# Kernel tuning notes

Measured on AMD Instinct MI355X. Metric: run time of the kernel, lower is better.

Reference implementation:

```python
import jax, jax.numpy as jnp
import numpy as np

N_NODES = 100000
N_EDGES = 800000
IN_DIM, HID_DIM, OUT_DIM = 128, 256, 40


def setup_inputs() -> dict:
    key = jax.random.key(0)
    ks = jax.random.split(key, 8)
    x = jax.random.normal(ks[0], (N_NODES, IN_DIM), dtype=jnp.float32)
    edge_index = jax.random.randint(ks[1], (2, N_EDGES), 0, N_NODES, dtype=jnp.int64)
    # PyG SAGEConv params: lin_l (neighbor path, with bias), lin_r (root path, no bias)
    def glorot(k, fan_in, fan_out):
        lim = np.sqrt(6.0 / (fan_in + fan_out)).astype(np.float32)
        return jax.random.uniform(k, (fan_in, fan_out), jnp.float32, -lim, lim)
    W1l = glorot(ks[2], IN_DIM, HID_DIM)
    W1r = glorot(ks[3], IN_DIM, HID_DIM)
    b1 = jnp.zeros((HID_DIM,), jnp.float32)
    W2l = glorot(ks[4], HID_DIM, OUT_DIM)
    W2r = glorot(ks[5], HID_DIM, OUT_DIM)
    b2 = jnp.zeros((OUT_DIM,), jnp.float32)
    return {"x": x, "edge_index": edge_index, "W1l": W1l, "b1": b1, "W1r": W1r,
            "W2l": W2l, "b2": b2, "W2r": W2r}


def _sage_conv(x, src, dst, Wl, b, Wr, n_nodes):
    # mean aggregation of neighbor features: gather x[src], scatter-add to dst, divide by degree
    msg = x[src]                                              # [E, D]
    agg = jax.ops.segment_sum(msg, dst, num_segments=n_nodes)  # [N, D]
    cnt = jax.ops.segment_sum(jnp.ones((src.shape[0],), x.dtype), dst,
                              num_segments=n_nodes)            # [N]
    agg = agg / jnp.maximum(cnt, 1.0)[:, None]
    # out = lin_l(mean_agg) + lin_r(x)  (lin_l carries the bias in PyG)
    return agg @ Wl + b + x @ Wr


def reference(x, edge_index, W1l, b1, W1r, W2l, b2, W2r):
    src, dst = edge_index[0], edge_index[1]
    n = x.shape[0]
    h = _sage_conv(x, src, dst, W1l, b1, W1r, n)
    h = jax.nn.relu(h)
    # F.dropout(training=self.training): identity at inference
    out = _sage_conv(h, src, dst, W2l, b2, W2r, n)
    return out
```

## Files before the change

### kernel.cpp

```cpp
#include <hip/hip_runtime.h>
#include <hip/hip_bf16.h>


#define NN   100000
#define NNP  100096
#define NE   800000
#define NB1  391
#define NCHK 32
#define ECH  25000
#define NSLI 16
#define NSL  6250

typedef unsigned short ushortT;
typedef __attribute__((ext_vector_type(8))) short bf16x8;
typedef __attribute__((ext_vector_type(4))) float f32x4;

__device__ __forceinline__ unsigned short f2b(float f) {
    unsigned u = __float_as_uint(f);
    return (unsigned short)((u + 0x7fffu + ((u >> 16) & 1u)) >> 16);
}
__device__ __forceinline__ float b2f(unsigned short v) {
    return __uint_as_float(((unsigned)v) << 16);
}
__device__ __forceinline__ void llds16(const unsigned short* g, unsigned short* s) {
    __builtin_amdgcn_global_load_lds(
        (const __attribute__((address_space(1))) void*)g,
        (__attribute__((address_space(3))) void*)s, 16, 0, 0);
}
__device__ __forceinline__ int fragIdx(int n, int k) {
    return (((n >> 4) * 8 + (k >> 5)) * 64 + ((k >> 3) & 3) * 16 + (n & 15)) * 8
           + (k & 7);
}

__global__ __launch_bounds__(256) void k_prep(
        const float* __restrict__ x,
        const float* __restrict__ W1l, const float* __restrict__ W1r,
        const float* __restrict__ W2l, const float* __restrict__ W2r,
        ushortT* __restrict__ Ac, ushortT* __restrict__ WT1f,
        ushortT* __restrict__ WT2f,
        const int* __restrict__ dst, int* __restrict__ deg32) {
    __shared__ int hist[NSL];
    int bid = blockIdx.x;
    if (bid < 12500) {
        int t = bid * 256 + threadIdx.x;
        int row = t >> 5, c4 = t & 31;
        float4 v = *(const float4*)&x[(size_t)row * 128 + c4 * 4];
        ushort4 o;
        o.x = f2b(v.x); o.y = f2b(v.y); o.z = f2b(v.z); o.w = f2b(v.w);
        *(ushort4*)(Ac + (size_t)row * 256 + 128 + c4 * 4) = o;

        if (t < 65536) {
            int n = t >> 8, k = t & 255;
            float w = (k < 128) ? W1l[(size_t)k * 256 + n]
                                : W1r[(size_t)(k - 128) * 256 + n];
            WT1f[fragIdx(n, k)] = f2b(w);
        } else if (t < 65536 + 20480) {
            int j = t - 65536;
            int n = j >> 8, k = j & 255;
            float w = (n < 40) ? W2l[(size_t)k * 40 + n]
                               : W2r[(size_t)k * 40 + (n - 40)];
            WT2f[fragIdx(n, k)] = f2b(w);
        }
    } else {
        int idx = bid - 12500;
        int s = idx & (NSLI - 1), c = idx >> 4;
        for (int i = threadIdx.x; i < NSL; i += 256) hist[i] = 0;
        __syncthreads();
        int e0 = c * ECH, lo = s * NSL;
        for (int i = threadIdx.x; i < ECH; i += 1024) {
            int d[4];
            bool m[4];
#pragma unroll
            for (int u = 0; u < 4; ++u) {
                int ii = i + u * 256;
                m[u] = ii < ECH;
                d[u] = dst[e0 + (m[u] ? ii : 0)];
            }
#pragma unroll
            for (int u = 0; u < 4; ++u) {
                unsigned dd = (unsigned)(d[u] - lo);
                if (m[u] && dd < (unsigned)NSL) atomicAdd(&hist[dd], 1);
            }
        }
        __syncthreads();
        for (int i = threadIdx.x; i < NSL; i += 256)
            deg32[c * NN + lo + i] = hist[i];
    }
}

__global__ __launch_bounds__(256) void k_scan1(const int* __restrict__ deg32,
                                               int* __restrict__ rp,
                                               int* __restrict__ rpp,
                                               int* __restrict__ bsum) {
    __shared__ int s[256];
    int t = threadIdx.x;
    int i = blockIdx.x * 256 + t;
    int d32[NCHK];
    int v = 0;
#pragma unroll
    for (int r = 0; r < NCHK; ++r) {
        d32[r] = (i < NN) ? deg32[r * NN + i] : 0;
        v += d32[r];
    }
    s[t] = v;
    __syncthreads();
    for (int off = 1; off < 256; off <<= 1) {
        int add = (t >= off) ? s[t - off] : 0;
        __syncthreads();
        s[t] += add;
        __syncthreads();
    }
    int ex = s[t] - v;
    if (i <= NN) rp[i] = ex;
    if (i < NN) {
        int run = ex;
#pragma unroll
        for (int r = 0; r < NCHK; ++r) {
            rpp[r * NN + i] = run;
            run += d32[r];
        }
    }
    if (t == 255) bsum[blockIdx.x] = s[255];
}

__global__ __launch_bounds__(512) void k_scan2(int* __restrict__ bsum) {
    __shared__ int s[512];
    int t = threadIdx.x;
    int v = (t < NB1) ? bsum[t] : 0;
    s[t] = v;
    __syncthreads();
    for (int off = 1; off < 512; off <<= 1) {
        int add = (t >= off) ? s[t - off] : 0;
        __syncthreads();
        s[t] += add;
        __syncthreads();
    }
    if (t < NB1) bsum[t] = s[t] - v;
}

__global__ __launch_bounds__(256) void k_fillB(const int* __restrict__ src,
                                               const int* __restrict__ dst,
                                               const int* __restrict__ rpp,
                                               const int* __restrict__ bsum,
                                               int* __restrict__ col) {
    __shared__ int off[NSL];
    int s = blockIdx.x & (NSLI - 1), c = blockIdx.x >> 4;
    int lo = s * NSL;
    for (int i = threadIdx.x; i < NSL; i += 256)
        off[i] = bsum[(lo + i) >> 8] + rpp[c * NN + lo + i];
    __syncthreads();
    int e0 = c * ECH;
    for (int i = threadIdx.x; i < ECH; i += 1024) {
        int d[4], sv[4];
        bool m[4];
#pragma unroll
        for (int u = 0; u < 4; ++u) {
            int ii = i + u * 256;
            m[u] = ii < ECH;
            int e = e0 + (m[u] ? ii : 0);
            d[u] = dst[e];
            sv[u] = src[e];
        }
#pragma unroll
        for (int u = 0; u < 4; ++u) {
            unsigned dd = (unsigned)(d[u] - lo);
            if (m[u] && dd < (unsigned)NSL) {
                int k = atomicAdd(&off[dd], 1);
                col[k] = sv[u];
            }
        }
    }
}

__global__ __launch_bounds__(256) void k_agg1(const int* __restrict__ rp,
                                              const int* __restrict__ bsum,
                                              const int* __restrict__ col,
                                              ushortT* __restrict__ Ac) {
    int node = blockIdx.x * 4 + (threadIdx.x >> 6);
    int l = threadIdx.x & 63;
    if (node >= NN) return;
    int seg = l >> 4, dl = l & 15;
    int beg = rp[node] + bsum[node >> 8];
    int end = rp[node + 1] + bsum[(node + 1) >> 8];
    int deg = end - beg;
    float a[8] = {0.f, 0.f, 0.f, 0.f, 0.f, 0.f, 0.f, 0.f};
    for (int base = 0; base < deg; base += 64) {
        int cnt = min(64, deg - base);
        int cv = col[beg + base + min(l, cnt - 1)];
        for (int j = 0; j < cnt; j += 16) {
            int e[4], idx[4];
            bf16x8 v[4];
#pragma unroll
            for (int u = 0; u < 4; ++u) {
                e[u] = j + u * 4 + seg;
                idx[u] = __shfl(cv, min(e[u], cnt - 1));
            }
#pragma unroll
            for (int u = 0; u < 4; ++u) {
                v[u] = (bf16x8){0, 0, 0, 0, 0, 0, 0, 0};
                if (e[u] < cnt)
                    v[u] = *(const bf16x8*)(Ac + (size_t)idx[u] * 256 + 128 + dl * 8);
            }
#pragma unroll
            for (int u = 0; u < 4; ++u)
#pragma unroll
                for (int i = 0; i < 8; ++i)
                    a[i] += b2f((unsigned short)v[u][i]);
        }
    }
#pragma unroll
    for (int i = 0; i < 8; ++i) {
        a[i] += __shfl_xor(a[i], 16);
        a[i] += __shfl_xor(a[i], 32);
    }
    if (seg == 0) {
        float inv = 1.0f / fmaxf((float)deg, 1.0f);
        bf16x8 o;
#pragma unroll
        for (int i = 0; i < 8; ++i) o[i] = (short)f2b(a[i] * inv);
        *(bf16x8*)(Ac + (size_t)node * 256 + dl * 8) = o;
    }
}

#define HSP 264
__global__ __launch_bounds__(256, 3) void k_fused(
        const ushortT* __restrict__ Ac, const ushortT* __restrict__ WT1f,
        const float* __restrict__ b1, const ushortT* __restrict__ WT2f,
        const float* __restrict__ b2, ushortT* __restrict__ y2,
        ushortT* __restrict__ t) {
    __shared__ ushortT Bs[64 * HSP];
    const int tid = threadIdx.x, l = tid & 63, wid = tid >> 6;
    const int m0 = blockIdx.x * 64;
    const int q = l >> 4, r = l & 15;
    const int swz = (l & 7) ^ ((l >> 3) & 7);

#pragma unroll
    for (int ktc = 0; ktc < 4; ++ktc)
#pragma unroll
        for (int i = 0; i < 2; ++i) {
            int flat = wid * 2 + i;
            int row = flat * 8 + (l >> 3);
            llds16(Ac + (size_t)(m0 + row) * 256 + ktc * 64 + swz * 8,
                   &Bs[ktc * 4096 + flat * 512]);
        }

    f32x4 acc[4][4];
#pragma unroll
    for (int i = 0; i < 4; ++i)
#pragma unroll
        for (int j = 0; j < 4; ++j) acc[i][j] = (f32x4){0.f, 0.f, 0.f, 0.f};

    __syncthreads();

    const ushortT* bBase = WT1f + (size_t)(wid * 4 * 8) * 512 + l * 8;
#pragma unroll
    for (int kk = 0; kk < 256; kk += 32) {
        const int ktc = kk >> 6, ks = kk & 63, kc = kk >> 5;
        const int cs = (((ks >> 3) + q) ^ (r & 7)) * 8;
        bf16x8 af[4], bfr[4];
#pragma unroll
        for (int mt = 0; mt < 4; ++mt)
            af[mt] = *(const bf16x8*)&Bs[ktc * 4096 + (mt * 16 + r) * 64 + cs];
#pragma unroll
        for (int nt = 0; nt < 4; ++nt)
            bfr[nt] = *(const bf16x8*)(bBase + (size_t)(nt * 8 + kc) * 512);
#pragma unroll
        for (int mt = 0; mt < 4; ++mt)
#pragma unroll
            for (int nt = 0; nt < 4; ++nt)
                acc[mt][nt] = __builtin_amdgcn_mfma_f32_16x16x32_bf16(
                    af[mt], bfr[nt], acc[mt][nt], 0, 0, 0);
    }
    __syncthreads();

#pragma unroll
    for (int nt = 0; nt < 4; ++nt) {
        int colb = wid * 64 + nt * 16 + r;
        float bb = b1[colb];
#pragma unroll
        for (int mt = 0; mt < 4; ++mt) {
            int rowb = mt * 16 + q * 4;
#pragma unroll
            for (int j = 0; j < 4; ++j)
                Bs[(rowb + j) * HSP + colb] = f2b(fmaxf(acc[mt][nt][j] + bb, 0.f));
        }
    }
    __syncthreads();

    f32x4 acc2[2][4];
#pragma unroll
    for (int i = 0; i < 2; ++i)
#pragma unroll
        for (int j = 0; j < 4; ++j) acc2[i][j] = (f32x4){0.f, 0.f, 0.f, 0.f};
#pragma unroll
    for (int kk = 0; kk < 256; kk += 32) {
        bf16x8 af[4];
#pragma unroll
        for (int mt = 0; mt < 4; ++mt)
            af[mt] = *(const bf16x8*)&Bs[(mt * 16 + r) * HSP + kk + q * 8];
#pragma unroll
        for (int cc = 0; cc < 2; ++cc) {
            int ct = wid + cc * 4;
            if (ct < 5) {
                bf16x8 bq = *(const bf16x8*)(WT2f
                        + (size_t)(ct * 8 + (kk >> 5)) * 512 + l * 8);
#pragma unroll
                for (int mt = 0; mt < 4; ++mt)
                    acc2[cc][mt] = __builtin_amdgcn_mfma_f32_16x16x32_bf16(
                        af[mt], bq, acc2[cc][mt], 0, 0, 0);
            }
        }
    }
#pragma unroll
    for (int cc = 0; cc < 2; ++cc) {
        int ct = wid + cc * 4;
        if (ct >= 5) continue;
        int c = ct * 16 + r;
        float bb = (c >= 40) ? b2[c - 40] : 0.f;
#pragma unroll
        for (int mt = 0; mt < 4; ++mt) {
            int row0 = m0 + mt * 16 + q * 4;
#pragma unroll
            for (int j = 0; j < 4; ++j) {
                float v = acc2[cc][mt][j];
                if (c < 40)
                    y2[(size_t)(row0 + j) * 40 + c] = f2b(v);
                else
                    t[(size_t)(row0 + j) * 40 + (c - 40)] = f2b(v + bb);
            }
        }
    }
}

__global__ __launch_bounds__(256) void k_agg2(const int* __restrict__ rp,
                                              const int* __restrict__ bsum,
                                              const int* __restrict__ col,
                                              const ushortT* __restrict__ y2,
                                              const ushortT* __restrict__ t,
                                              float* __restrict__ out) {
    int node = blockIdx.x * 4 + (threadIdx.x >> 6);
    int l = threadIdx.x & 63;
    if (node >= NN) return;
    int seg = l >> 4, dl = l & 15;
    int beg = rp[node] + bsum[node >> 8];
    int end = rp[node + 1] + bsum[(node + 1) >> 8];
    int deg = end - beg;
    bool act = dl < 10;
    float a0 = 0.f, a1 = 0.f, a2 = 0.f, a3 = 0.f;
    for (int base = 0; base < deg; base += 64) {
        int cnt = min(64, deg - base);
        int cv = col[beg + base + min(l, cnt - 1)];
        for (int j = 0; j < cnt; j += 16) {
            int e[4], idx[4];
            ushort4 v[4];
#pragma unroll
            for (int u = 0; u < 4; ++u) {
                e[u] = j + u * 4 + seg;
                idx[u] = __shfl(cv, min(e[u], cnt - 1));
            }
#pragma unroll
            for (int u = 0; u < 4; ++u) {
                v[u] = (ushort4){0, 0, 0, 0};
                if (e[u] < cnt && act)
                    v[u] = *(const ushort4*)(y2 + (size_t)idx[u] * 40 + dl * 4);
            }
#pragma unroll
            for (int u = 0; u < 4; ++u) {
                a0 += b2f(v[u].x);
                a1 += b2f(v[u].y);
                a2 += b2f(v[u].z);
                a3 += b2f(v[u].w);
            }
        }
    }
    a0 += __shfl_xor(a0, 16); a0 += __shfl_xor(a0, 32);
    a1 += __shfl_xor(a1, 16); a1 += __shfl_xor(a1, 32);
    a2 += __shfl_xor(a2, 16); a2 += __shfl_xor(a2, 32);
    a3 += __shfl_xor(a3, 16); a3 += __shfl_xor(a3, 32);
    if (seg == 0 && act) {
        float inv = 1.0f / fmaxf((float)deg, 1.0f);
        size_t o = (size_t)node * 40 + dl * 4;
        ushort4 tv = *(const ushort4*)&t[o];
        float4 ov;
        ov.x = a0 * inv + b2f(tv.x);
        ov.y = a1 * inv + b2f(tv.y);
        ov.z = a2 * inv + b2f(tv.z);
        ov.w = a3 * inv + b2f(tv.w);
        *(float4*)&out[o] = ov;
    }
}

extern "C" void kernel_launch(void* const* d_in, const int* in_sizes, int n_in,
                              void* d_out, int out_size, void* d_ws, size_t ws_size,
                              hipStream_t stream) {
    const float* x   = (const float*)d_in[0];
    const int*   ei  = (const int*)d_in[1];
    const int*   src = ei;
    const int*   dst = ei + NE;
    const float* W1l = (const float*)d_in[2];
    const float* b1  = (const float*)d_in[3];
    const float* W1r = (const float*)d_in[4];
    const float* W2l = (const float*)d_in[5];
    const float* b2  = (const float*)d_in[6];
    const float* W2r = (const float*)d_in[7];
    float* out = (float*)d_out;

    size_t off = 0;
    char* base = (char*)d_ws;
    auto alloc = [&](size_t bytes) -> void* {
        void* p = base + off;
        off += (bytes + 255) & ~(size_t)255;
        return p;
    };
    int*     deg32 = (int*)alloc((size_t)NCHK * NN * 4);
    int*     rp    = (int*)alloc((size_t)(NN + 1) * 4);
    int*     rpp   = (int*)alloc((size_t)NCHK * NN * 4);
    int*     col   = (int*)alloc((size_t)NE * 4);
    int*     bsum  = (int*)alloc(512 * 4);
    ushortT* Ac    = (ushortT*)alloc((size_t)NNP * 256 * 2);
    ushortT* y2    = (ushortT*)alloc((size_t)NNP * 40 * 2);
    ushortT* t     = (ushortT*)alloc((size_t)NNP * 40 * 2);
    ushortT* WT1f  = (ushortT*)alloc(256 * 256 * 2);
    ushortT* WT2f  = (ushortT*)alloc(80 * 256 * 2);

    k_prep<<<12500 + NCHK * NSLI, 256, 0, stream>>>(x, W1l, W1r, W2l, W2r,
                                                    Ac, WT1f, WT2f, dst, deg32);
    k_scan1<<<NB1, 256, 0, stream>>>(deg32, rp, rpp, bsum);
    k_scan2<<<1, 512, 0, stream>>>(bsum);
    k_fillB<<<NCHK * NSLI, 256, 0, stream>>>(src, dst, rpp, bsum, col);
    k_agg1<<<(NN + 3) / 4, 256, 0, stream>>>(rp, bsum, col, Ac);
    k_fused<<<NNP / 64, 256, 0, stream>>>(Ac, WT1f, b1, WT2f, b2, y2, t);
    k_agg2<<<(NN + 3) / 4, 256, 0, stream>>>(rp, bsum, col, y2, t, out);
}
```

Before: 272.0 us.

## Use 8 waves per block in fused GEMM with double-buffered fragment loads

Doubles the fused GEMM block to 512 threads, splitting the 64-row tile into 2x4 wave tiles of 32x64 instead of four 64x64 wave tiles, which roughly halves per-wave accumulator registers. The first GEMM's K loop now software-pipelines LDS and global fragment loads with ping-pong register buffers, and the second GEMM gives each of the first five waves one output column tile. The goal is more latency hiding and occupancy. The trade-off is that each wave reloads B fragments with less reuse, and three of the eight waves sit idle during the second GEMM.

```diff
diff --git a/kernel.cpp b/kernel.cpp
--- a/kernel.cpp
+++ b/kernel.cpp
@@ -223,7 +223,31 @@
 }
 
 #define HSP 264
-__global__ __launch_bounds__(256, 3) void k_fused(
+
+#define LD_A(dst, kkv) {                                                     \
+    const int ktc_ = (kkv) >> 6, ks_ = (kkv) & 63;                           \
+    const int cs_ = (((ks_ >> 3) + q) ^ (r & 7)) * 8;                        \
+    _Pragma("unroll")                                                        \
+    for (int mt = 0; mt < 2; ++mt)                                           \
+        dst[mt] = *(const bf16x8*)&Bs[ktc_ * 4096 +                          \
+                                      (wm * 32 + mt * 16 + r) * 64 + cs_];   \
+}
+#define LD_B(dst, kkv) {                                                     \
+    const int kc_ = (kkv) >> 5;                                              \
+    _Pragma("unroll")                                                        \
+    for (int nt = 0; nt < 4; ++nt)                                           \
+        dst[nt] = *(const bf16x8*)(bBase + (size_t)(nt * 8 + kc_) * 512);    \
+}
+#define DO_MFMA(afX, bfX) {                                                  \
+    _Pragma("unroll")                                                        \
+    for (int mt = 0; mt < 2; ++mt)                                           \
+        _Pragma("unroll")                                                    \
+        for (int nt = 0; nt < 4; ++nt)                                       \
+            acc[mt][nt] = __builtin_amdgcn_mfma_f32_16x16x32_bf16(           \
+                afX[mt], bfX[nt], acc[mt][nt], 0, 0, 0);                     \
+}
+
+__global__ __launch_bounds__(512, 4) void k_fused(
         const ushortT* __restrict__ Ac, const ushortT* __restrict__ WT1f,
         const float* __restrict__ b1, const ushortT* __restrict__ WT2f,
         const float* __restrict__ b2, ushortT* __restrict__ y2,
@@ -233,53 +257,48 @@
     const int m0 = blockIdx.x * 64;
     const int q = l >> 4, r = l & 15;
     const int swz = (l & 7) ^ ((l >> 3) & 7);
-
-#pragma unroll
-    for (int ktc = 0; ktc < 4; ++ktc)
-#pragma unroll
-        for (int i = 0; i < 2; ++i) {
-            int flat = wid * 2 + i;
-            int row = flat * 8 + (l >> 3);
-            llds16(Ac + (size_t)(m0 + row) * 256 + ktc * 64 + swz * 8,
-                   &Bs[ktc * 4096 + flat * 512]);
-        }
-
-    f32x4 acc[4][4];
-#pragma unroll
-    for (int i = 0; i < 4; ++i)
+    const int wm = wid >> 2;
+    const int wn = wid & 3;
+
+#pragma unroll
+    for (int i = 0; i < 4; ++i) {
+        int idx = wid * 4 + i;
+        int ktc = idx >> 3, flat = idx & 7;
+        int row = flat * 8 + (l >> 3);
+        llds16(Ac + (size_t)(m0 + row) * 256 + ktc * 64 + swz * 8,
+               &Bs[ktc * 4096 + flat * 512]);
+    }
+
+    f32x4 acc[2][4];
+#pragma unroll
+    for (int i = 0; i < 2; ++i)
 #pragma unroll
         for (int j = 0; j < 4; ++j) acc[i][j] = (f32x4){0.f, 0.f, 0.f, 0.f};
 
     __syncthreads();
 
-    const ushortT* bBase = WT1f + (size_t)(wid * 4 * 8) * 512 + l * 8;
-#pragma unroll
-    for (int kk = 0; kk < 256; kk += 32) {
-        const int ktc = kk >> 6, ks = kk & 63, kc = kk >> 5;
-        const int cs = (((ks >> 3) + q) ^ (r & 7)) * 8;
-        bf16x8 af[4], bfr[4];
-#pragma unroll
-        for (int mt = 0; mt < 4; ++mt)
-            af[mt] = *(const bf16x8*)&Bs[ktc * 4096 + (mt * 16 + r) * 64 + cs];
-#pragma unroll
-        for (int nt = 0; nt < 4; ++nt)
-            bfr[nt] = *(const bf16x8*)(bBase + (size_t)(nt * 8 + kc) * 512);
-#pragma unroll
-        for (int mt = 0; mt < 4; ++mt)
-#pragma unroll
-            for (int nt = 0; nt < 4; ++nt)
-                acc[mt][nt] = __builtin_amdgcn_mfma_f32_16x16x32_bf16(
-                    af[mt], bfr[nt], acc[mt][nt], 0, 0, 0);
-    }
+    const ushortT* bBase = WT1f + (size_t)(wn * 32) * 512 + l * 8;
+    bf16x8 afA[2], afB[2], bfrA[4], bfrB[4];
+    LD_A(afA, 0); LD_B(bfrA, 0);
+#pragma unroll
+    for (int s = 0; s < 3; ++s) {
+        LD_A(afB, s * 64 + 32); LD_B(bfrB, s * 64 + 32);
+        DO_MFMA(afA, bfrA);
+        LD_A(afA, s * 64 + 64); LD_B(bfrA, s * 64 + 64);
+        DO_MFMA(afB, bfrB);
+    }
+    LD_A(afB, 224); LD_B(bfrB, 224);
+    DO_MFMA(afA, bfrA);
+    DO_MFMA(afB, bfrB);
     __syncthreads();
 
 #pragma unroll
     for (int nt = 0; nt < 4; ++nt) {
-        int colb = wid * 64 + nt * 16 + r;
+        int colb = wn * 64 + nt * 16 + r;
         float bb = b1[colb];
 #pragma unroll
-        for (int mt = 0; mt < 4; ++mt) {
-            int rowb = mt * 16 + q * 4;
+        for (int mt = 0; mt < 2; ++mt) {
+            int rowb = wm * 32 + mt * 16 + q * 4;
 #pragma unroll
             for (int j = 0; j < 4; ++j)
                 Bs[(rowb + j) * HSP + colb] = f2b(fmaxf(acc[mt][nt][j] + bb, 0.f));
@@ -287,42 +306,31 @@
     }
     __syncthreads();
 
-    f32x4 acc2[2][4];
-#pragma unroll
-    for (int i = 0; i < 2; ++i)
-#pragma unroll
-        for (int j = 0; j < 4; ++j) acc2[i][j] = (f32x4){0.f, 0.f, 0.f, 0.f};
-#pragma unroll
-    for (int kk = 0; kk < 256; kk += 32) {
-        bf16x8 af[4];
-#pragma unroll
-        for (int mt = 0; mt < 4; ++mt)
-            af[mt] = *(const bf16x8*)&Bs[(mt * 16 + r) * HSP + kk + q * 8];
-#pragma unroll
-        for (int cc = 0; cc < 2; ++cc) {
-            int ct = wid + cc * 4;
-            if (ct < 5) {
-                bf16x8 bq = *(const bf16x8*)(WT2f
-                        + (size_t)(ct * 8 + (kk >> 5)) * 512 + l * 8);
-#pragma unroll
-                for (int mt = 0; mt < 4; ++mt)
-                    acc2[cc][mt] = __builtin_amdgcn_mfma_f32_16x16x32_bf16(
-                        af[mt], bq, acc2[cc][mt], 0, 0, 0);
-            }
-        }
-    }
-#pragma unroll
-    for (int cc = 0; cc < 2; ++cc) {
-        int ct = wid + cc * 4;
-        if (ct >= 5) continue;
-        int c = ct * 16 + r;
+    if (wid < 5) {
+        f32x4 acc2[4];
+#pragma unroll
+        for (int j = 0; j < 4; ++j) acc2[j] = (f32x4){0.f, 0.f, 0.f, 0.f};
+#pragma unroll
+        for (int kk = 0; kk < 256; kk += 32) {
+            bf16x8 af2[4];
+#pragma unroll
+            for (int mt = 0; mt < 4; ++mt)
+                af2[mt] = *(const bf16x8*)&Bs[(mt * 16 + r) * HSP + kk + q * 8];
+            bf16x8 bq = *(const bf16x8*)(WT2f
+                    + (size_t)(wid * 8 + (kk >> 5)) * 512 + l * 8);
+#pragma unroll
+            for (int mt = 0; mt < 4; ++mt)
+                acc2[mt] = __builtin_amdgcn_mfma_f32_16x16x32_bf16(
+                    af2[mt], bq, acc2[mt], 0, 0, 0);
+        }
+        int c = wid * 16 + r;
         float bb = (c >= 40) ? b2[c - 40] : 0.f;
 #pragma unroll
         for (int mt = 0; mt < 4; ++mt) {
             int row0 = m0 + mt * 16 + q * 4;
 #pragma unroll
             for (int j = 0; j < 4; ++j) {
-                float v = acc2[cc][mt][j];
+                float v = acc2[mt][j];
                 if (c < 40)
                     y2[(size_t)(row0 + j) * 40 + c] = f2b(v);
                 else
@@ -429,6 +437,6 @@
     k_scan2<<<1, 512, 0, stream>>>(bsum);
     k_fillB<<<NCHK * NSLI, 256, 0, stream>>>(src, dst, rpp, bsum, col);
     k_agg1<<<(NN + 3) / 4, 256, 0, stream>>>(rp, bsum, col, Ac);
-    k_fused<<<NNP / 64, 256, 0, stream>>>(Ac, WT1f, b1, WT2f, b2, y2, t);
+    k_fused<<<NNP / 64, 512, 0, stream>>>(Ac, WT1f, b1, WT2f, b2, y2, t);
     k_agg2<<<(NN + 3) / 4, 256, 0, stream>>>(rp, bsum, col, y2, t, out);
 }
```

After: 272.4 us. No clear change (+0.2%).

## Use 8 waves per block in fused MLP kernel and prefetch weights into registers

Applied to the files above, without the earlier changes.

The fused two-layer GEMM kernel now runs 512 threads (8 wavefronts) per 64-row tile instead of 4. Each wave computes 32 output columns of layer 1, and 5 of the 8 waves compute one 16-column tile of layer 2. All layer-1 and layer-2 weight fragments and biases are loaded into registers before the first barrier, so global weight loads overlap the LDS fill. This is meant to raise MFMA parallelism and hide weight-load latency, at the cost of more registers per thread and 3 of 8 waves idling in the second GEMM.

```diff
diff --git a/kernel.cpp b/kernel.cpp
--- a/kernel.cpp
+++ b/kernel.cpp
@@ -223,7 +223,7 @@
 }
 
 #define HSP 264
-__global__ __launch_bounds__(256, 3) void k_fused(
+__global__ __launch_bounds__(512, 3) void k_fused(
         const ushortT* __restrict__ Ac, const ushortT* __restrict__ WT1f,
         const float* __restrict__ b1, const ushortT* __restrict__ WT2f,
         const float* __restrict__ b2, ushortT* __restrict__ y2,
@@ -235,98 +235,102 @@
     const int swz = (l & 7) ^ ((l >> 3) & 7);
 
 #pragma unroll
-    for (int ktc = 0; ktc < 4; ++ktc)
-#pragma unroll
-        for (int i = 0; i < 2; ++i) {
-            int flat = wid * 2 + i;
-            int row = flat * 8 + (l >> 3);
-            llds16(Ac + (size_t)(m0 + row) * 256 + ktc * 64 + swz * 8,
-                   &Bs[ktc * 4096 + flat * 512]);
-        }
-
-    f32x4 acc[4][4];
+    for (int i = 0; i < 4; ++i) {
+        int idx = wid * 4 + i;
+        int ktc = idx >> 3, flat = idx & 7;
+        int row = flat * 8 + (l >> 3);
+        llds16(Ac + (size_t)(m0 + row) * 256 + ktc * 64 + swz * 8,
+               &Bs[ktc * 4096 + flat * 512]);
+    }
+
+    const ushortT* bBase = WT1f + (size_t)(wid * 16) * 512 + l * 8;
+    bf16x8 bfr[16];
+#pragma unroll
+    for (int kc = 0; kc < 8; ++kc)
+#pragma unroll
+        for (int nt = 0; nt < 2; ++nt)
+            bfr[kc * 2 + nt] = *(const bf16x8*)(bBase + (size_t)(nt * 8 + kc) * 512);
+
+    float bb1[2];
+#pragma unroll
+    for (int nt = 0; nt < 2; ++nt) bb1[nt] = b1[wid * 32 + nt * 16 + r];
+
+    f32x4 acc[4][2];
 #pragma unroll
     for (int i = 0; i < 4; ++i)
 #pragma unroll
-        for (int j = 0; j < 4; ++j) acc[i][j] = (f32x4){0.f, 0.f, 0.f, 0.f};
-
-    __syncthreads();
-
-    const ushortT* bBase = WT1f + (size_t)(wid * 4 * 8) * 512 + l * 8;
-#pragma unroll
-    for (int kk = 0; kk < 256; kk += 32) {
-        const int ktc = kk >> 6, ks = kk & 63, kc = kk >> 5;
+        for (int j = 0; j < 2; ++j) acc[i][j] = (f32x4){0.f, 0.f, 0.f, 0.f};
+
+    __syncthreads();
+
+#pragma unroll
+    for (int kc = 0; kc < 8; ++kc) {
+        const int ktc = kc >> 1, ks = (kc & 1) * 32;
         const int cs = (((ks >> 3) + q) ^ (r & 7)) * 8;
-        bf16x8 af[4], bfr[4];
+        bf16x8 af[4];
 #pragma unroll
         for (int mt = 0; mt < 4; ++mt)
             af[mt] = *(const bf16x8*)&Bs[ktc * 4096 + (mt * 16 + r) * 64 + cs];
 #pragma unroll
-        for (int nt = 0; nt < 4; ++nt)
-            bfr[nt] = *(const bf16x8*)(bBase + (size_t)(nt * 8 + kc) * 512);
-#pragma unroll
         for (int mt = 0; mt < 4; ++mt)
 #pragma unroll
-            for (int nt = 0; nt < 4; ++nt)
+            for (int nt = 0; nt < 2; ++nt)
                 acc[mt][nt] = __builtin_amdgcn_mfma_f32_16x16x32_bf16(
-                    af[mt], bfr[nt], acc[mt][nt], 0, 0, 0);
-    }
-    __syncthreads();
-
-#pragma unroll
-    for (int nt = 0; nt < 4; ++nt) {
-        int colb = wid * 64 + nt * 16 + r;
-        float bb = b1[colb];
+                    af[mt], bfr[kc * 2 + nt], acc[mt][nt], 0, 0, 0);
+    }
+
+    bf16x8 bq[8];
+    float bb2 = 0.f;
+    if (wid < 5) {
+#pragma unroll
+        for (int kc = 0; kc < 8; ++kc)
+            bq[kc] = *(const bf16x8*)(WT2f + (size_t)(wid * 8 + kc) * 512 + l * 8);
+        int c = wid * 16 + r;
+        if (c >= 40) bb2 = b2[c - 40];
+    }
+
+    __syncthreads();
+
+#pragma unroll
+    for (int nt = 0; nt < 2; ++nt) {
+        int colb = wid * 32 + nt * 16 + r;
 #pragma unroll
         for (int mt = 0; mt < 4; ++mt) {
             int rowb = mt * 16 + q * 4;
 #pragma unroll
             for (int j = 0; j < 4; ++j)
-                Bs[(rowb + j) * HSP + colb] = f2b(fmaxf(acc[mt][nt][j] + bb, 0.f));
-        }
-    }
-    __syncthreads();
-
-    f32x4 acc2[2][4];
-#pragma unroll
-    for (int i = 0; i < 2; ++i)
-#pragma unroll
-        for (int j = 0; j < 4; ++j) acc2[i][j] = (f32x4){0.f, 0.f, 0.f, 0.f};
-#pragma unroll
-    for (int kk = 0; kk < 256; kk += 32) {
-        bf16x8 af[4];
-#pragma unroll
-        for (int mt = 0; mt < 4; ++mt)
-            af[mt] = *(const bf16x8*)&Bs[(mt * 16 + r) * HSP + kk + q * 8];
-#pragma unroll
-        for (int cc = 0; cc < 2; ++cc) {
-            int ct = wid + cc * 4;
-            if (ct < 5) {
-                bf16x8 bq = *(const bf16x8*)(WT2f
-                        + (size_t)(ct * 8 + (kk >> 5)) * 512 + l * 8);
-#pragma unroll
-                for (int mt = 0; mt < 4; ++mt)
-                    acc2[cc][mt] = __builtin_amdgcn_mfma_f32_16x16x32_bf16(
-                        af[mt], bq, acc2[cc][mt], 0, 0, 0);
-            }
-        }
-    }
-#pragma unroll
-    for (int cc = 0; cc < 2; ++cc) {
-        int ct = wid + cc * 4;
-        if (ct >= 5) continue;
-        int c = ct * 16 + r;
-        float bb = (c >= 40) ? b2[c - 40] : 0.f;
+                Bs[(rowb + j) * HSP + colb] =
+                    f2b(fmaxf(acc[mt][nt][j] + bb1[nt], 0.f));
+        }
+    }
+    __syncthreads();
+
+    if (wid < 5) {
+        f32x4 acc2[4];
+#pragma unroll
+        for (int j = 0; j < 4; ++j) acc2[j] = (f32x4){0.f, 0.f, 0.f, 0.f};
+#pragma unroll
+        for (int kc = 0; kc < 8; ++kc) {
+            bf16x8 af2[4];
+#pragma unroll
+            for (int mt = 0; mt < 4; ++mt)
+                af2[mt] = *(const bf16x8*)&Bs[(mt * 16 + r) * HSP + kc * 32 + q * 8];
+#pragma unroll
+            for (int mt = 0; mt < 4; ++mt)
+                acc2[mt] = __builtin_amdgcn_mfma_f32_16x16x32_bf16(
+                    af2[mt], bq[kc], acc2[mt], 0, 0, 0);
+        }
+        int c = wid * 16 + r;
 #pragma unroll
         for (int mt = 0; mt < 4; ++mt) {
             int row0 = m0 + mt * 16 + q * 4;
 #pragma unroll
             for (int j = 0; j < 4; ++j) {
-                float v = acc2[cc][mt][j];
+                float v = acc2[mt][j];
                 if (c < 40)
                     y2[(size_t)(row0 + j) * 40 + c] = f2b(v);
                 else
-                    t[(size_t)(row0 + j) * 40 + (c - 40)] = f2b(v + bb);
+                    t[(size_t)(row0 + j) * 40 + (c - 40)] = f2b(v + bb2);
             }
         }
     }
@@ -429,6 +433,6 @@
     k_scan2<<<1, 512, 0, stream>>>(bsum);
     k_fillB<<<NCHK * NSLI, 256, 0, stream>>>(src, dst, rpp, bsum, col);
     k_agg1<<<(NN + 3) / 4, 256, 0, stream>>>(rp, bsum, col, Ac);
-    k_fused<<<NNP / 64, 256, 0, stream>>>(Ac, WT1f, b1, WT2f, b2, y2, t);
+    k_fused<<<NNP / 64, 512, 0, stream>>>(Ac, WT1f, b1, WT2f, b2, y2, t);
     k_agg2<<<(NN + 3) / 4, 256, 0, stream>>>(rp, bsum, col, y2, t, out);
 }
```

Measured after the change: 263.4 us. 1.03x faster.
